# Kernel tuning notes

Measured on AMD Instinct MI355X. Metric: run time of the kernel, lower is better.

## Reference

```python
import jax, jax.numpy as jnp
import numpy as np

N_NODES = 50000
N_EDGES = 800000
N_GRAPHS = 64
NEG_SLOPE = 0.2
EPS = 1e-16


def _gat_layer(x, src, dst, W, b, att_l, att_r):
    H, C = att_l.shape
    n = x.shape[0]
    # lin_l == lin_r (shared weights in the source module)
    xl = (x @ W.T + b).reshape(n, H, C)            # [N,H,C]
    alpha_l = jnp.sum(xl * att_l, axis=-1)         # [N,H]
    alpha_r = jnp.sum(xl * att_r, axis=-1)         # [N,H]
    # per-edge attention logits: alpha_i (dst) + alpha_j (src)
    e = jax.nn.leaky_relu(alpha_r[dst] + alpha_l[src], NEG_SLOPE)  # [E,H]
    # segment softmax over destination node
    m = jax.ops.segment_max(e, dst, num_segments=n)
    e = jnp.exp(e - m[dst])
    denom = jax.ops.segment_sum(e, dst, num_segments=n)
    alpha = e / (denom[dst] + EPS)                 # [E,H]
    msg = xl[src] * alpha[:, :, None]              # [E,H,C]
    out = jax.ops.segment_sum(msg, dst, num_segments=n)  # [N,H,C]
    return out.reshape(n, H * C)


def setup_inputs() -> dict:
    key = jax.random.key(0)
    ks = jax.random.split(key, 10)
    x = jax.random.normal(ks[0], (N_NODES, 128), dtype=jnp.float32)
    edge_index = jax.random.randint(ks[1], (2, N_EDGES), 0, N_NODES, dtype=jnp.int32)
    batch = jnp.sort(jax.random.randint(ks[2], (N_NODES,), 0, N_GRAPHS, dtype=jnp.int32))
    s = 1.0 / np.sqrt(128.0)
    Ws = jax.random.normal(ks[3], (3, 128, 128), dtype=jnp.float32) * s
    bs = jnp.zeros((3, 128), dtype=jnp.float32)
    att_ls = jax.random.normal(ks[4], (3, 4, 32), dtype=jnp.float32) * s
    att_rs = jax.random.normal(ks[5], (3, 4, 32), dtype=jnp.float32) * s
    proj_W = jax.random.normal(ks[6], (32, 128), dtype=jnp.float32) * s
    proj_b = jnp.zeros((32,), dtype=jnp.float32)
    return {"x": x, "edge_index": edge_index, "batch": batch, "Ws": Ws, "bs": bs,
            "att_ls": att_ls, "att_rs": att_rs, "proj_W": proj_W, "proj_b": proj_b}


def reference(x, edge_index, batch, Ws, bs, att_ls, att_rs, proj_W, proj_b):
    src, dst = edge_index[0], edge_index[1]
    h = x
    for l in range(3):
        h = _gat_layer(h, src, dst, Ws[l], bs[l], att_ls[l], att_rs[l])
        h = jax.nn.relu(h)  # dropout disabled (eval mode)
    pooled = jax.ops.segment_sum(h, batch, num_segments=N_GRAPHS)  # [G, H*C]
    return pooled @ proj_W.T + proj_b  # output_dim=None -> return embedding
```

## Files before the change

kernel.cpp:

```cpp
#include <hip/hip_runtime.h>
#include <hip/hip_bf16.h>

#define NHEADS 4
#define DIM 128
#define NEG_SLOPE 0.2f
#define POOL_CHUNK 256

typedef __bf16 bf16x8 __attribute__((ext_vector_type(8)));
typedef float  f32x4  __attribute__((ext_vector_type(4)));

__device__ __forceinline__ float lrelu(float x) { return x > 0.f ? x : NEG_SLOPE * x; }
__device__ __forceinline__ float bf2f(unsigned short u) {
    return __uint_as_float(((unsigned)u) << 16);
}
__device__ __forceinline__ unsigned short f2bf(float f) {
    __bf16 b = (__bf16)f;
    return __builtin_bit_cast(unsigned short, b);
}
__device__ __forceinline__ float4 lrelu4(float4 a, float4 b) {
    return make_float4(lrelu(a.x + b.x), lrelu(a.y + b.y), lrelu(a.z + b.z), lrelu(a.w + b.w));
}
__device__ __forceinline__ float4 redmax4(float4 v) {
#pragma unroll
    for (int off = 32; off >= 1; off >>= 1) {
        v.x = fmaxf(v.x, __shfl_xor(v.x, off));
        v.y = fmaxf(v.y, __shfl_xor(v.y, off));
        v.z = fmaxf(v.z, __shfl_xor(v.z, off));
        v.w = fmaxf(v.w, __shfl_xor(v.w, off));
    }
    return v;
}
__device__ __forceinline__ float4 redsum4(float4 v) {
#pragma unroll
    for (int off = 32; off >= 1; off >>= 1) {
        v.x += __shfl_xor(v.x, off);
        v.y += __shfl_xor(v.y, off);
        v.z += __shfl_xor(v.z, off);
        v.w += __shfl_xor(v.w, off);
    }
    return v;
}

__global__ __launch_bounds__(256) void pack_w(
    const float* __restrict__ Ws, __bf16* __restrict__ Wb, int total)
{
    int o = blockIdx.x * 256 + threadIdx.x;
    if (o >= total) return;
    int layer = o >> 14;
    int t = o & 16383;
    int j = t & 7, l = (t >> 3) & 63, kk = (t >> 9) & 3, g = t >> 11;
    int col = g * 16 + (l & 15);
    int k = kk * 32 + (l >> 4) * 8 + j;
    Wb[o] = (__bf16)Ws[(size_t)layer * 16384 + col * 128 + k];
}

template<bool ABF>
__device__ __forceinline__ void gemm_body(
    const float* __restrict__ inF, const unsigned short* __restrict__ inB,
    const uint4* __restrict__ Wb4, const float* __restrict__ bias,
    const float* __restrict__ attl, const float* __restrict__ attr,
    __bf16* __restrict__ xlb, float* __restrict__ al, float* __restrict__ ar,
    int n, int bid)
{
    const int tid = threadIdx.x;
    const int wid = tid >> 6, l = tid & 63;
    const int rowA = bid * 64 + wid * 16 + (l & 15);
    const int kchunk = (l >> 4) * 8;

    f32x4 acc[8];
#pragma unroll
    for (int g = 0; g < 8; ++g)
#pragma unroll
        for (int r = 0; r < 4; ++r) acc[g][r] = 0.f;

#pragma unroll
    for (int kk = 0; kk < 4; ++kk) {
        bf16x8 afrag;
        if (ABF) {
            uint4 u = make_uint4(0, 0, 0, 0);
            if (rowA < n)
                u = *(const uint4*)(inB + (size_t)rowA * DIM + kk * 32 + kchunk);
            afrag = __builtin_bit_cast(bf16x8, u);
        } else {
            float av[8];
            if (rowA < n) {
                const float* p = inF + (size_t)rowA * DIM + kk * 32 + kchunk;
                float4 x0 = *(const float4*)p;
                float4 x1 = *(const float4*)(p + 4);
                av[0]=x0.x; av[1]=x0.y; av[2]=x0.z; av[3]=x0.w;
                av[4]=x1.x; av[5]=x1.y; av[6]=x1.z; av[7]=x1.w;
            } else {
#pragma unroll
                for (int i = 0; i < 8; ++i) av[i] = 0.f;
            }
#pragma unroll
            for (int i = 0; i < 8; ++i) afrag[i] = (__bf16)av[i];
        }
#pragma unroll
        for (int g = 0; g < 8; ++g) {
            uint4 u = Wb4[(g * 4 + kk) * 64 + l];
            bf16x8 bfrag = __builtin_bit_cast(bf16x8, u);
            acc[g] = __builtin_amdgcn_mfma_f32_16x16x32_bf16(afrag, bfrag, acc[g], 0, 0, 0);
        }
    }

    const int rowbase = bid * 64 + wid * 16 + (l >> 4) * 4;
    float pl[4][4], pr2[4][4];
#pragma unroll
    for (int r = 0; r < 4; ++r)
#pragma unroll
        for (int h = 0; h < 4; ++h) { pl[r][h] = 0.f; pr2[r][h] = 0.f; }

#pragma unroll
    for (int g = 0; g < 8; ++g) {
        int col = g * 16 + (l & 15);
        float bg = bias[col], alg = attl[col], arg = attr[col];
        int h = g >> 1;
#pragma unroll
        for (int r = 0; r < 4; ++r) {
            float v = acc[g][r] + bg;
            int row = rowbase + r;
            if (row < n) xlb[(size_t)row * DIM + col] = (__bf16)v;
            pl[r][h]  = fmaf(v, alg, pl[r][h]);
            pr2[r][h] = fmaf(v, arg, pr2[r][h]);
        }
    }
#pragma unroll
    for (int off = 1; off <= 8; off <<= 1) {
#pragma unroll
        for (int r = 0; r < 4; ++r)
#pragma unroll
            for (int h = 0; h < 4; ++h) {
                pl[r][h]  += __shfl_xor(pl[r][h], off);
                pr2[r][h] += __shfl_xor(pr2[r][h], off);
            }
    }
    if ((l & 15) == 0) {
#pragma unroll
        for (int r = 0; r < 4; ++r) {
            int row = rowbase + r;
            if (row < n) {
#pragma unroll
                for (int h = 0; h < 4; ++h) {
                    al[row * 4 + h] = pl[r][h];
                    ar[row * 4 + h] = pr2[r][h];
                }
            }
        }
    }
}

template<bool ABF>
__global__ __launch_bounds__(256) void gemm_mfma(
    const float* __restrict__ inF, const unsigned short* __restrict__ inB,
    const uint4* __restrict__ Wb4, const float* __restrict__ bias,
    const float* __restrict__ attl, const float* __restrict__ attr,
    __bf16* __restrict__ xlb, float* __restrict__ al, float* __restrict__ ar, int n)
{
    gemm_body<ABF>(inF, inB, Wb4, bias, attl, attr, xlb, al, ar, n, blockIdx.x);
}

__global__ __launch_bounds__(256) void gemm0_classify(
    const float* __restrict__ inF, const uint4* __restrict__ Wb4,
    const float* __restrict__ bias,
    const float* __restrict__ attl, const float* __restrict__ attr,
    __bf16* __restrict__ xlb, float* __restrict__ al, float* __restrict__ ar,
    int n, int gemmBlocks,
    const int* __restrict__ src, const int* __restrict__ dst,
    int* __restrict__ bwpos, unsigned* __restrict__ ebuf, int E)
{
    if ((int)blockIdx.x < gemmBlocks) {
        gemm_body<false>(inF, nullptr, Wb4, bias, attl, attr, xlb, al, ar, n, blockIdx.x);
    } else {
        __shared__ unsigned stage[4096];
        __shared__ unsigned char sid[4096];
        __shared__ int hist[256], lofs[256], wofs[256], gbase[256];
        int t = threadIdx.x;
        int e0 = (blockIdx.x - gemmBlocks) * 4096;
        int cnt = min(4096, E - e0);
        if (cnt <= 0) return;
        hist[t] = 0;
        __syncthreads();
        for (int k = t; k < cnt; k += 256)
            atomicAdd(&hist[dst[e0 + k] >> 8], 1);
        __syncthreads();
        int v = hist[t];
        lofs[t] = v;
        __syncthreads();
        int val = v;
        for (int off = 1; off < 256; off <<= 1) {
            int other = (t >= off) ? lofs[t - off] : 0;
            __syncthreads();
            val += other;
            lofs[t] = val;
            __syncthreads();
        }
        int excl = val - v;
        int gb_ = (v > 0) ? atomicAdd(&bwpos[t], v) : 0;
        lofs[t] = excl; wofs[t] = excl; gbase[t] = gb_;
        __syncthreads();
        for (int k = t; k < cnt; k += 256) {
            int d = dst[e0 + k], s = src[e0 + k];
            int b = d >> 8;
            int slot = atomicAdd(&wofs[b], 1);
            stage[slot] = (unsigned)(s & 0xffff) | ((unsigned)(d & 255) << 16);
            sid[slot] = (unsigned char)b;
        }
        __syncthreads();
        for (int s_ = t; s_ < cnt; s_ += 256) {
            int b = sid[s_];
            ebuf[gbase[b] + (s_ - lofs[b])] = stage[s_];
        }
    }
}

__global__ __launch_bounds__(256) void bucket_rank(
    const unsigned* __restrict__ ebuf, const int* __restrict__ rowptr,
    int* __restrict__ col, int n)
{
    __shared__ int wp[256];
    int nb0 = blockIdx.x << 8;
    int t = threadIdx.x;
    int nend = min(nb0 + 256, n);
    int base = rowptr[nb0];
    int eend = rowptr[nend];
    if (nb0 + t < nend) wp[t] = rowptr[nb0 + t] - base;
    __syncthreads();
    for (int e = base + t; e < eend; e += 256) {
        unsigned ed = ebuf[e];
        int r = atomicAdd(&wp[(ed >> 16) & 255], 1);
        col[base + r] = (int)(ed & 0xffffu);
    }
}

__global__ __launch_bounds__(256) void deg_count(
    const int* __restrict__ dst, int* __restrict__ deg, int E)
{
    int e = blockIdx.x * blockDim.x + threadIdx.x;
    if (e < E) atomicAdd(&deg[dst[e]], 1);
}

__global__ __launch_bounds__(256) void scan_blocks(
    const int* __restrict__ deg, int* __restrict__ rowptr,
    int* __restrict__ partials, int n)
{
    __shared__ int tot[256];
    int t = threadIdx.x;
    int base = blockIdx.x * 1024 + t * 4;
    int v[4];
#pragma unroll
    for (int j = 0; j < 4; ++j) v[j] = (base + j < n) ? deg[base + j] : 0;
    int p1 = v[0], p2 = p1 + v[1], p3 = p2 + v[2], sum4 = p3 + v[3];
    tot[t] = sum4;
    __syncthreads();
    int val = sum4;
    for (int off = 1; off < 256; off <<= 1) {
        int other = (t >= off) ? tot[t - off] : 0;
        __syncthreads();
        val += other;
        tot[t] = val;
        __syncthreads();
    }
    int excl = val - sum4;
    if (base < n)     rowptr[base]     = excl;
    if (base+1 < n)   rowptr[base+1]   = excl + p1;
    if (base+2 < n)   rowptr[base+2]   = excl + p2;
    if (base+3 < n)   rowptr[base+3]   = excl + p3;
    if (t == 255) partials[blockIdx.x] = val;
}

__global__ __launch_bounds__(256) void scan_partials(
    int* __restrict__ partials, int nb, int* __restrict__ rowptr, int n)
{
    __shared__ int tot[256];
    int t = threadIdx.x;
    int v = (t < nb) ? partials[t] : 0;
    tot[t] = v;
    __syncthreads();
    int val = v;
    for (int off = 1; off < 256; off <<= 1) {
        int other = (t >= off) ? tot[t - off] : 0;
        __syncthreads();
        val += other;
        tot[t] = val;
        __syncthreads();
    }
    if (t < nb) partials[t] = val - v;
    if (t == 255) rowptr[n] = val;
}

__global__ __launch_bounds__(256) void add_offsets(
    int* __restrict__ rowptr, int* __restrict__ bwpos,
    const int* __restrict__ partials, int n)
{
    int base = blockIdx.x * 1024 + threadIdx.x * 4;
    int off = partials[blockIdx.x];
#pragma unroll
    for (int j = 0; j < 4; ++j) {
        int i = base + j;
        if (i < n) {
            int r = rowptr[i] + off;
            rowptr[i] = r;
            if ((i & 255) == 0) bwpos[i >> 8] = r;
        }
    }
}

__device__ __forceinline__ void agg_chunk2(
    const int* __restrict__ slds, const float* __restrict__ wl,
    int cn, int q, const unsigned short* __restrict__ xp,
    f32x4& A, f32x4& B, f32x4& C, f32x4& D)
{
    int i = 0;
    for (; i + 8 <= cn; i += 8) {
        int e0 = i + q, e1 = i + 2 + q, e2 = i + 4 + q, e3 = i + 6 + q;
        int s0 = slds[e0], s1 = slds[e1], s2 = slds[e2], s3 = slds[e3];
        float w0 = wl[e0*4], w1 = wl[e1*4], w2 = wl[e2*4], w3 = wl[e3*4];
        ushort4 v0 = *(const ushort4*)(xp + (size_t)s0 * DIM);
        ushort4 v1 = *(const ushort4*)(xp + (size_t)s1 * DIM);
        ushort4 v2 = *(const ushort4*)(xp + (size_t)s2 * DIM);
        ushort4 v3 = *(const ushort4*)(xp + (size_t)s3 * DIM);
        A[0] = fmaf(w0, bf2f(v0.x), A[0]); A[1] = fmaf(w0, bf2f(v0.y), A[1]);
        A[2] = fmaf(w0, bf2f(v0.z), A[2]); A[3] = fmaf(w0, bf2f(v0.w), A[3]);
        B[0] = fmaf(w1, bf2f(v1.x), B[0]); B[1] = fmaf(w1, bf2f(v1.y), B[1]);
        B[2] = fmaf(w1, bf2f(v1.z), B[2]); B[3] = fmaf(w1, bf2f(v1.w), B[3]);
        C[0] = fmaf(w2, bf2f(v2.x), C[0]); C[1] = fmaf(w2, bf2f(v2.y), C[1]);
        C[2] = fmaf(w2, bf2f(v2.z), C[2]); C[3] = fmaf(w2, bf2f(v2.w), C[3]);
        D[0] = fmaf(w3, bf2f(v3.x), D[0]); D[1] = fmaf(w3, bf2f(v3.y), D[1]);
        D[2] = fmaf(w3, bf2f(v3.z), D[2]); D[3] = fmaf(w3, bf2f(v3.w), D[3]);
    }
    for (; i < cn; i += 2) {
        int e = i + q;
        if (e < cn) {
            int s = slds[e];
            float w = wl[e*4];
            ushort4 v = *(const ushort4*)(xp + (size_t)s * DIM);
            A[0] = fmaf(w, bf2f(v.x), A[0]); A[1] = fmaf(w, bf2f(v.y), A[1]);
            A[2] = fmaf(w, bf2f(v.z), A[2]); A[3] = fmaf(w, bf2f(v.w), A[3]);
        }
    }
}

__global__ __launch_bounds__(256) void gat_aggregate(
    const int* __restrict__ rowptr, const int* __restrict__ col,
    const float* __restrict__ al, const float* __restrict__ ar,
    const unsigned short* __restrict__ xlb, unsigned short* __restrict__ outb, int n)
{
    __shared__ float4 wlds[4][64];
    __shared__ int    slds[4][64];
    int wid = threadIdx.x >> 6;
    int node = blockIdx.x * 4 + wid;
    if (node >= n) return;
    int lane = threadIdx.x & 63;
    int q = lane >> 5, c32 = lane & 31;
    int h = c32 >> 3;
    int r0 = rowptr[node], r1 = rowptr[node + 1];
    int deg = r1 - r0;
    unsigned short* po = outb + (size_t)node * DIM + c32 * 4;
    if (deg == 0) {
        if (q == 0) *(ushort4*)po = make_ushort4(0, 0, 0, 0);
        return;
    }

    float4 arv = *(const float4*)(ar + (size_t)node * 4);
    const float* wl = (const float*)&wlds[wid][0] + h;
    const unsigned short* xp = xlb + c32 * 4;
    f32x4 A = {0.f,0.f,0.f,0.f}, B = {0.f,0.f,0.f,0.f};
    f32x4 C = {0.f,0.f,0.f,0.f}, D = {0.f,0.f,0.f,0.f};
    float4 inv4;

    if (deg <= 64) {
        float4 l4 = make_float4(-1e30f, -1e30f, -1e30f, -1e30f);
        int s = 0;
        if (lane < deg) {
            s = col[r0 + lane];
            float4 a = *(const float4*)(al + (size_t)s * 4);
            l4 = lrelu4(arv, a);
        }
        float4 m4 = redmax4(l4);
        float4 p4 = make_float4(0.f, 0.f, 0.f, 0.f);
        if (lane < deg) {
            p4.x = __expf(l4.x - m4.x); p4.y = __expf(l4.y - m4.y);
            p4.z = __expf(l4.z - m4.z); p4.w = __expf(l4.w - m4.w);
        }
        float4 s4 = redsum4(p4);
        inv4 = make_float4(1.f/(s4.x+1e-16f), 1.f/(s4.y+1e-16f),
                           1.f/(s4.z+1e-16f), 1.f/(s4.w+1e-16f));
        if (lane < deg) { wlds[wid][lane] = p4; slds[wid][lane] = s; }
        __asm__ volatile("s_waitcnt lgkmcnt(0)" ::: "memory");
        __builtin_amdgcn_sched_barrier(0);
        agg_chunk2(&slds[wid][0], wl, deg, q, xp, A, B, C, D);
    } else {
        float4 m4 = make_float4(-1e30f, -1e30f, -1e30f, -1e30f);
        for (int i = lane; i < deg; i += 64) {
            int s = col[r0 + i];
            float4 a = *(const float4*)(al + (size_t)s * 4);
            float4 t = lrelu4(arv, a);
            m4.x = fmaxf(m4.x, t.x); m4.y = fmaxf(m4.y, t.y);
            m4.z = fmaxf(m4.z, t.z); m4.w = fmaxf(m4.w, t.w);
        }
        m4 = redmax4(m4);
        float4 s4 = make_float4(0.f, 0.f, 0.f, 0.f);
        for (int i = lane; i < deg; i += 64) {
            int s = col[r0 + i];
            float4 a = *(const float4*)(al + (size_t)s * 4);
            float4 t = lrelu4(arv, a);
            s4.x += __expf(t.x - m4.x); s4.y += __expf(t.y - m4.y);
            s4.z += __expf(t.z - m4.z); s4.w += __expf(t.w - m4.w);
        }
        s4 = redsum4(s4);
        inv4 = make_float4(1.f/(s4.x+1e-16f), 1.f/(s4.y+1e-16f),
                           1.f/(s4.z+1e-16f), 1.f/(s4.w+1e-16f));
        for (int c0 = 0; c0 < deg; c0 += 64) {
            int cn = min(64, deg - c0);
            if (lane < cn) {
                int s = col[r0 + c0 + lane];
                float4 a = *(const float4*)(al + (size_t)s * 4);
                float4 t = lrelu4(arv, a);
                float4 p;
                p.x = __expf(t.x - m4.x); p.y = __expf(t.y - m4.y);
                p.z = __expf(t.z - m4.z); p.w = __expf(t.w - m4.w);
                wlds[wid][lane] = p; slds[wid][lane] = s;
            }
            __asm__ volatile("s_waitcnt lgkmcnt(0)" ::: "memory");
            __builtin_amdgcn_sched_barrier(0);
            agg_chunk2(&slds[wid][0], wl, cn, q, xp, A, B, C, D);
            __asm__ volatile("s_waitcnt lgkmcnt(0)" ::: "memory");
            __builtin_amdgcn_sched_barrier(0);
        }
    }
    float invh = (h == 0) ? inv4.x : (h == 1) ? inv4.y : (h == 2) ? inv4.z : inv4.w;
    f32x4 T;
#pragma unroll
    for (int j = 0; j < 4; ++j) {
        T[j] = A[j] + B[j] + C[j] + D[j];
        T[j] += __shfl_xor(T[j], 32);
    }
    if (q == 0) {
        ushort4 o4;
        o4.x = f2bf(fmaxf(T[0] * invh, 0.f));
        o4.y = f2bf(fmaxf(T[1] * invh, 0.f));
        o4.z = f2bf(fmaxf(T[2] * invh, 0.f));
        o4.w = f2bf(fmaxf(T[3] * invh, 0.f));
        *(ushort4*)po = o4;
    }
}

__global__ __launch_bounds__(256) void pool_nodes_seg(
    const unsigned short* __restrict__ h, const int* __restrict__ batch,
    float* __restrict__ pooled, int n)
{
    int wid = threadIdx.x >> 6;
    int lane = threadIdx.x & 63;
    int start = blockIdx.x * POOL_CHUNK;
    int end = min(start + POOL_CHUNK, n);
    float a0 = 0.f, a1 = 0.f;
    int curg = -1;
    for (int node = start + wid; node < end; node += 4) {
        int g = batch[node];
        if (g != curg) {
            if (curg >= 0) {
                unsafeAtomicAdd(pooled + (size_t)curg * DIM + lane*2,     a0);
                unsafeAtomicAdd(pooled + (size_t)curg * DIM + lane*2 + 1, a1);
            }
            curg = g; a0 = 0.f; a1 = 0.f;
        }
        ushort2 v = *(const ushort2*)(h + (size_t)node * DIM + lane * 2);
        a0 += bf2f(v.x);
        a1 += bf2f(v.y);
    }
    if (curg >= 0) {
        unsafeAtomicAdd(pooled + (size_t)curg * DIM + lane*2,     a0);
        unsafeAtomicAdd(pooled + (size_t)curg * DIM + lane*2 + 1, a1);
    }
}

__global__ __launch_bounds__(256) void proj_out(
    const float* __restrict__ pooled, const float* __restrict__ W,
    const float* __restrict__ b, float* __restrict__ out, int G)
{
    int idx = blockIdx.x * blockDim.x + threadIdx.x;
    if (idx >= G * 32) return;
    int g = idx >> 5, j = idx & 31;
    const float* pr = pooled + (size_t)g * DIM;
    const float* wr = W + (size_t)j * DIM;
    float acc = 0.f;
#pragma unroll
    for (int k = 0; k < DIM; ++k) acc = fmaf(pr[k], wr[k], acc);
    out[idx] = acc + b[j];
}

extern "C" void kernel_launch(void* const* d_in, const int* in_sizes, int n_in,
                              void* d_out, int out_size, void* d_ws, size_t ws_size,
                              hipStream_t stream)
{
    const float* x      = (const float*)d_in[0];
    const int*   eidx   = (const int*)d_in[1];
    const int*   batch  = (const int*)d_in[2];
    const float* Ws     = (const float*)d_in[3];
    const float* bs     = (const float*)d_in[4];
    const float* attls  = (const float*)d_in[5];
    const float* attrs  = (const float*)d_in[6];
    const float* projW  = (const float*)d_in[7];
    const float* projb  = (const float*)d_in[8];

    const int N = in_sizes[0] / DIM;
    const int E = in_sizes[1] / 2;
    const int G = out_size / 32;
    const int* src = eidx;
    const int* dst = eidx + E;

    char* ws = (char*)d_ws;
    size_t o = 0;
    auto alloc = [&](size_t bytes) { char* p = ws + o; o += (bytes + 255) & ~255ull; return p; };
    unsigned short* hA  = (unsigned short*)alloc((size_t)N * DIM * 2);
    unsigned short* hB  = (unsigned short*)alloc((size_t)N * DIM * 2);
    __bf16* xlb    = (__bf16*)alloc((size_t)N * DIM * 2);
    float*  al     = (float*)alloc((size_t)N * 4 * 4);
    float*  ar     = (float*)alloc((size_t)N * 4 * 4);
    int*    rowptr = (int*)alloc((size_t)(N + 1) * 4);
    int*    deg    = (int*)alloc((size_t)N * 4);
    int*    colv   = (int*)alloc((size_t)E * 4);
    unsigned* ebuf = (unsigned*)alloc((size_t)E * 4);
    int*    bwpos  = (int*)alloc((size_t)((N + 255) / 256) * 4);
    int*    parts  = (int*)alloc(256 * 4);
    float*  pooled = (float*)alloc((size_t)G * DIM * 4);
    __bf16* Wb     = (__bf16*)alloc((size_t)3 * 16384 * 2);

    const int wtot = 3 * 16384;
    pack_w<<<(wtot + 255) / 256, 256, 0, stream>>>(Ws, Wb, wtot);

    const int nb = (N + 1023) / 1024;
    hipMemsetAsync(deg, 0, (size_t)N * 4, stream);
    deg_count<<<(E + 255) / 256, 256, 0, stream>>>(dst, deg, E);
    scan_blocks<<<nb, 256, 0, stream>>>(deg, rowptr, parts, N);
    scan_partials<<<1, 256, 0, stream>>>(parts, nb, rowptr, N);
    add_offsets<<<nb, 256, 0, stream>>>(rowptr, bwpos, parts, N);

    const int gb = (N + 63) / 64;
    const int cb = (E + 4095) / 4096;
    const int rb = (N + 255) / 256;

    gemm0_classify<<<gb + cb, 256, 0, stream>>>(
        x, (const uint4*)Wb, bs, attls, attrs, xlb, al, ar, N, gb,
        src, dst, bwpos, ebuf, E);
    bucket_rank<<<rb, 256, 0, stream>>>(ebuf, rowptr, colv, N);
    gat_aggregate<<<(N + 3) / 4, 256, 0, stream>>>(rowptr, colv, al, ar,
        (const unsigned short*)xlb, hA, N);

    const unsigned short* hin = hA;
    unsigned short* houts[2] = {hB, hA};
    for (int l = 1; l < 3; ++l) {
        unsigned short* hout = houts[l - 1];
        const uint4* Wb4 = (const uint4*)(Wb + (size_t)l * 16384);
        gemm_mfma<true><<<gb, 256, 0, stream>>>(nullptr, hin, Wb4, bs + l*DIM,
            attls + l*DIM, attrs + l*DIM, xlb, al, ar, N);
        gat_aggregate<<<(N + 3) / 4, 256, 0, stream>>>(rowptr, colv, al, ar,
            (const unsigned short*)xlb, hout, N);
        hin = hout;
    }

    hipMemsetAsync(pooled, 0, (size_t)G * DIM * 4, stream);
    pool_nodes_seg<<<(N + POOL_CHUNK - 1) / POOL_CHUNK, 256, 0, stream>>>(hA, batch, pooled, N);
    proj_out<<<(G * 32 + 255) / 256, 256, 0, stream>>>(pooled, projW, projb, (float*)d_out, G);
}
```

Baseline: 293.3 us.

## Drop softmax max pass, widen aggregation loads, fuse weight packing with degree count

Removes the per-node max reduction from the segment softmax and exponentiates raw logits directly, eliminating a shuffle reduction and an extra edge pass for high-degree nodes. The aggregation loop now has each lane load 8 bf16 features (16-byte loads) across 4 edge groups instead of 4 features across 2. Weight packing and degree counting are merged into one launch. Skipping the max subtraction risks exp overflow for large attention logits.

New measurement: 258.6 us. 1.13x faster.

```diff
diff --git a/kernel.cpp b/kernel.cpp
--- a/kernel.cpp
+++ b/kernel.cpp
@@ -17,18 +17,11 @@
     __bf16 b = (__bf16)f;
     return __builtin_bit_cast(unsigned short, b);
 }
+__device__ __forceinline__ unsigned pack2bf(float a, float b) {
+    return (unsigned)f2bf(a) | ((unsigned)f2bf(b) << 16);
+}
 __device__ __forceinline__ float4 lrelu4(float4 a, float4 b) {
     return make_float4(lrelu(a.x + b.x), lrelu(a.y + b.y), lrelu(a.z + b.z), lrelu(a.w + b.w));
-}
-__device__ __forceinline__ float4 redmax4(float4 v) {
-#pragma unroll
-    for (int off = 32; off >= 1; off >>= 1) {
-        v.x = fmaxf(v.x, __shfl_xor(v.x, off));
-        v.y = fmaxf(v.y, __shfl_xor(v.y, off));
-        v.z = fmaxf(v.z, __shfl_xor(v.z, off));
-        v.w = fmaxf(v.w, __shfl_xor(v.w, off));
-    }
-    return v;
 }
 __device__ __forceinline__ float4 redsum4(float4 v) {
 #pragma unroll
@@ -39,19 +32,6 @@
         v.w += __shfl_xor(v.w, off);
     }
     return v;
-}
-
-__global__ __launch_bounds__(256) void pack_w(
-    const float* __restrict__ Ws, __bf16* __restrict__ Wb, int total)
-{
-    int o = blockIdx.x * 256 + threadIdx.x;
-    if (o >= total) return;
-    int layer = o >> 14;
-    int t = o & 16383;
-    int j = t & 7, l = (t >> 3) & 63, kk = (t >> 9) & 3, g = t >> 11;
-    int col = g * 16 + (l & 15);
-    int k = kk * 32 + (l >> 4) * 8 + j;
-    Wb[o] = (__bf16)Ws[(size_t)layer * 16384 + col * 128 + k];
 }
 
 template<bool ABF>
@@ -233,11 +213,23 @@
     }
 }
 
-__global__ __launch_bounds__(256) void deg_count(
+__global__ __launch_bounds__(256) void prep_pack_deg(
+    const float* __restrict__ Ws, __bf16* __restrict__ Wb, int wtot, int wb,
     const int* __restrict__ dst, int* __restrict__ deg, int E)
 {
-    int e = blockIdx.x * blockDim.x + threadIdx.x;
-    if (e < E) atomicAdd(&deg[dst[e]], 1);
+    if ((int)blockIdx.x < wb) {
+        int o = blockIdx.x * 256 + threadIdx.x;
+        if (o >= wtot) return;
+        int layer = o >> 14;
+        int t = o & 16383;
+        int j = t & 7, l = (t >> 3) & 63, kk = (t >> 9) & 3, g = t >> 11;
+        int col = g * 16 + (l & 15);
+        int k = kk * 32 + (l >> 4) * 8 + j;
+        Wb[o] = (__bf16)Ws[(size_t)layer * 16384 + col * 128 + k];
+    } else {
+        int e = (blockIdx.x - wb) * 256 + threadIdx.x;
+        if (e < E) atomicAdd(&deg[dst[e]], 1);
+    }
 }
 
 __global__ __launch_bounds__(256) void scan_blocks(
@@ -306,37 +298,41 @@
     }
 }
 
-__device__ __forceinline__ void agg_chunk2(
+__device__ __forceinline__ void acc_edge(
+    uint4 v, float w, f32x4& lo, f32x4& hi)
+{
+    lo[0] = fmaf(w, __uint_as_float(v.x << 16), lo[0]);
+    lo[1] = fmaf(w, __uint_as_float(v.x & 0xffff0000u), lo[1]);
+    lo[2] = fmaf(w, __uint_as_float(v.y << 16), lo[2]);
+    lo[3] = fmaf(w, __uint_as_float(v.y & 0xffff0000u), lo[3]);
+    hi[0] = fmaf(w, __uint_as_float(v.z << 16), hi[0]);
+    hi[1] = fmaf(w, __uint_as_float(v.z & 0xffff0000u), hi[1]);
+    hi[2] = fmaf(w, __uint_as_float(v.w << 16), hi[2]);
+    hi[3] = fmaf(w, __uint_as_float(v.w & 0xffff0000u), hi[3]);
+}
+
+__device__ __forceinline__ void agg_chunk4w(
     const int* __restrict__ slds, const float* __restrict__ wl,
-    int cn, int q, const unsigned short* __restrict__ xp,
-    f32x4& A, f32x4& B, f32x4& C, f32x4& D)
+    int cn, int eg, const unsigned short* __restrict__ xp,
+    f32x4& A0, f32x4& A1, f32x4& B0, f32x4& B1)
 {
     int i = 0;
     for (; i + 8 <= cn; i += 8) {
-        int e0 = i + q, e1 = i + 2 + q, e2 = i + 4 + q, e3 = i + 6 + q;
-        int s0 = slds[e0], s1 = slds[e1], s2 = slds[e2], s3 = slds[e3];
-        float w0 = wl[e0*4], w1 = wl[e1*4], w2 = wl[e2*4], w3 = wl[e3*4];
-        ushort4 v0 = *(const ushort4*)(xp + (size_t)s0 * DIM);
-        ushort4 v1 = *(const ushort4*)(xp + (size_t)s1 * DIM);
-        ushort4 v2 = *(const ushort4*)(xp + (size_t)s2 * DIM);
-        ushort4 v3 = *(const ushort4*)(xp + (size_t)s3 * DIM);
-        A[0] = fmaf(w0, bf2f(v0.x), A[0]); A[1] = fmaf(w0, bf2f(v0.y), A[1]);
-        A[2] = fmaf(w0, bf2f(v0.z), A[2]); A[3] = fmaf(w0, bf2f(v0.w), A[3]);
-        B[0] = fmaf(w1, bf2f(v1.x), B[0]); B[1] = fmaf(w1, bf2f(v1.y), B[1]);
-        B[2] = fmaf(w1, bf2f(v1.z), B[2]); B[3] = fmaf(w1, bf2f(v1.w), B[3]);
-        C[0] = fmaf(w2, bf2f(v2.x), C[0]); C[1] = fmaf(w2, bf2f(v2.y), C[1]);
-        C[2] = fmaf(w2, bf2f(v2.z), C[2]); C[3] = fmaf(w2, bf2f(v2.w), C[3]);
-        D[0] = fmaf(w3, bf2f(v3.x), D[0]); D[1] = fmaf(w3, bf2f(v3.y), D[1]);
-        D[2] = fmaf(w3, bf2f(v3.z), D[2]); D[3] = fmaf(w3, bf2f(v3.w), D[3]);
-    }
-    for (; i < cn; i += 2) {
-        int e = i + q;
+        int e0 = i + eg, e1 = i + 4 + eg;
+        int s0 = slds[e0], s1 = slds[e1];
+        float w0 = wl[e0*4], w1 = wl[e1*4];
+        uint4 v0 = *(const uint4*)(xp + (size_t)s0 * DIM);
+        uint4 v1 = *(const uint4*)(xp + (size_t)s1 * DIM);
+        acc_edge(v0, w0, A0, A1);
+        acc_edge(v1, w1, B0, B1);
+    }
+    for (; i < cn; i += 4) {
+        int e = i + eg;
         if (e < cn) {
             int s = slds[e];
             float w = wl[e*4];
-            ushort4 v = *(const ushort4*)(xp + (size_t)s * DIM);
-            A[0] = fmaf(w, bf2f(v.x), A[0]); A[1] = fmaf(w, bf2f(v.y), A[1]);
-            A[2] = fmaf(w, bf2f(v.z), A[2]); A[3] = fmaf(w, bf2f(v.w), A[3]);
+            uint4 v = *(const uint4*)(xp + (size_t)s * DIM);
+            acc_edge(v, w, A0, A1);
         }
     }
 }
@@ -352,36 +348,31 @@
     int node = blockIdx.x * 4 + wid;
     if (node >= n) return;
     int lane = threadIdx.x & 63;
-    int q = lane >> 5, c32 = lane & 31;
-    int h = c32 >> 3;
+    int eg = lane >> 4, c16 = lane & 15;
+    int h = c16 >> 2;
     int r0 = rowptr[node], r1 = rowptr[node + 1];
     int deg = r1 - r0;
-    unsigned short* po = outb + (size_t)node * DIM + c32 * 4;
+    unsigned short* po = outb + (size_t)node * DIM + c16 * 8;
     if (deg == 0) {
-        if (q == 0) *(ushort4*)po = make_ushort4(0, 0, 0, 0);
+        if (eg == 0) *(uint4*)po = make_uint4(0, 0, 0, 0);
         return;
     }
 
     float4 arv = *(const float4*)(ar + (size_t)node * 4);
     const float* wl = (const float*)&wlds[wid][0] + h;
-    const unsigned short* xp = xlb + c32 * 4;
-    f32x4 A = {0.f,0.f,0.f,0.f}, B = {0.f,0.f,0.f,0.f};
-    f32x4 C = {0.f,0.f,0.f,0.f}, D = {0.f,0.f,0.f,0.f};
+    const unsigned short* xp = xlb + c16 * 8;
+    f32x4 A0 = {0,0,0,0}, A1 = {0,0,0,0}, B0 = {0,0,0,0}, B1 = {0,0,0,0};
     float4 inv4;
 
     if (deg <= 64) {
-        float4 l4 = make_float4(-1e30f, -1e30f, -1e30f, -1e30f);
+        float4 p4 = make_float4(0.f, 0.f, 0.f, 0.f);
         int s = 0;
         if (lane < deg) {
             s = col[r0 + lane];
             float4 a = *(const float4*)(al + (size_t)s * 4);
-            l4 = lrelu4(arv, a);
-        }
-        float4 m4 = redmax4(l4);
-        float4 p4 = make_float4(0.f, 0.f, 0.f, 0.f);
-        if (lane < deg) {
-            p4.x = __expf(l4.x - m4.x); p4.y = __expf(l4.y - m4.y);
-            p4.z = __expf(l4.z - m4.z); p4.w = __expf(l4.w - m4.w);
+            float4 l4 = lrelu4(arv, a);
+            p4.x = __expf(l4.x); p4.y = __expf(l4.y);
+            p4.z = __expf(l4.z); p4.w = __expf(l4.w);
         }
         float4 s4 = redsum4(p4);
         inv4 = make_float4(1.f/(s4.x+1e-16f), 1.f/(s4.y+1e-16f),
@@ -389,24 +380,15 @@
         if (lane < deg) { wlds[wid][lane] = p4; slds[wid][lane] = s; }
         __asm__ volatile("s_waitcnt lgkmcnt(0)" ::: "memory");
         __builtin_amdgcn_sched_barrier(0);
-        agg_chunk2(&slds[wid][0], wl, deg, q, xp, A, B, C, D);
+        agg_chunk4w(&slds[wid][0], wl, deg, eg, xp, A0, A1, B0, B1);
     } else {
-        float4 m4 = make_float4(-1e30f, -1e30f, -1e30f, -1e30f);
-        for (int i = lane; i < deg; i += 64) {
-            int s = col[r0 + i];
-            float4 a = *(const float4*)(al + (size_t)s * 4);
-            float4 t = lrelu4(arv, a);
-            m4.x = fmaxf(m4.x, t.x); m4.y = fmaxf(m4.y, t.y);
-            m4.z = fmaxf(m4.z, t.z); m4.w = fmaxf(m4.w, t.w);
-        }
-        m4 = redmax4(m4);
         float4 s4 = make_float4(0.f, 0.f, 0.f, 0.f);
         for (int i = lane; i < deg; i += 64) {
             int s = col[r0 + i];
             float4 a = *(const float4*)(al + (size_t)s * 4);
             float4 t = lrelu4(arv, a);
-            s4.x += __expf(t.x - m4.x); s4.y += __expf(t.y - m4.y);
-            s4.z += __expf(t.z - m4.z); s4.w += __expf(t.w - m4.w);
+            s4.x += __expf(t.x); s4.y += __expf(t.y);
+            s4.z += __expf(t.z); s4.w += __expf(t.w);
         }
         s4 = redsum4(s4);
         inv4 = make_float4(1.f/(s4.x+1e-16f), 1.f/(s4.y+1e-16f),
@@ -418,31 +400,32 @@
                 float4 a = *(const float4*)(al + (size_t)s * 4);
                 float4 t = lrelu4(arv, a);
                 float4 p;
-                p.x = __expf(t.x - m4.x); p.y = __expf(t.y - m4.y);
-                p.z = __expf(t.z - m4.z); p.w = __expf(t.w - m4.w);
+                p.x = __expf(t.x); p.y = __expf(t.y);
+                p.z = __expf(t.z); p.w = __expf(t.w);
                 wlds[wid][lane] = p; slds[wid][lane] = s;
             }
             __asm__ volatile("s_waitcnt lgkmcnt(0)" ::: "memory");
             __builtin_amdgcn_sched_barrier(0);
-            agg_chunk2(&slds[wid][0], wl, cn, q, xp, A, B, C, D);
+            agg_chunk4w(&slds[wid][0], wl, cn, eg, xp, A0, A1, B0, B1);
             __asm__ volatile("s_waitcnt lgkmcnt(0)" ::: "memory");
             __builtin_amdgcn_sched_barrier(0);
         }
     }
     float invh = (h == 0) ? inv4.x : (h == 1) ? inv4.y : (h == 2) ? inv4.z : inv4.w;
-    f32x4 T;
 #pragma unroll
     for (int j = 0; j < 4; ++j) {
-        T[j] = A[j] + B[j] + C[j] + D[j];
-        T[j] += __shfl_xor(T[j], 32);
-    }
-    if (q == 0) {
-        ushort4 o4;
-        o4.x = f2bf(fmaxf(T[0] * invh, 0.f));
-        o4.y = f2bf(fmaxf(T[1] * invh, 0.f));
-        o4.z = f2bf(fmaxf(T[2] * invh, 0.f));
-        o4.w = f2bf(fmaxf(T[3] * invh, 0.f));
-        *(ushort4*)po = o4;
+        A0[j] += B0[j];
+        A1[j] += B1[j];
+        A0[j] += __shfl_xor(A0[j], 16); A0[j] += __shfl_xor(A0[j], 32);
+        A1[j] += __shfl_xor(A1[j], 16); A1[j] += __shfl_xor(A1[j], 32);
+    }
+    if (eg == 0) {
+        uint4 o4;
+        o4.x = pack2bf(fmaxf(A0[0]*invh, 0.f), fmaxf(A0[1]*invh, 0.f));
+        o4.y = pack2bf(fmaxf(A0[2]*invh, 0.f), fmaxf(A0[3]*invh, 0.f));
+        o4.z = pack2bf(fmaxf(A1[0]*invh, 0.f), fmaxf(A1[1]*invh, 0.f));
+        o4.w = pack2bf(fmaxf(A1[2]*invh, 0.f), fmaxf(A1[3]*invh, 0.f));
+        *(uint4*)po = o4;
     }
 }
 
@@ -528,11 +511,12 @@
     __bf16* Wb     = (__bf16*)alloc((size_t)3 * 16384 * 2);
 
     const int wtot = 3 * 16384;
-    pack_w<<<(wtot + 255) / 256, 256, 0, stream>>>(Ws, Wb, wtot);
+    const int wb = (wtot + 255) / 256;
+    const int db = (E + 255) / 256;
+    hipMemsetAsync(deg, 0, (size_t)N * 4, stream);
+    prep_pack_deg<<<wb + db, 256, 0, stream>>>(Ws, Wb, wtot, wb, dst, deg, E);
 
     const int nb = (N + 1023) / 1024;
-    hipMemsetAsync(deg, 0, (size_t)N * 4, stream);
-    deg_count<<<(E + 255) / 256, 256, 0, stream>>>(dst, deg, E);
     scan_blocks<<<nb, 256, 0, stream>>>(deg, rowptr, parts, N);
     scan_partials<<<1, 256, 0, stream>>>(parts, nb, rowptr, N);
     add_offsets<<<nb, 256, 0, stream>>>(rowptr, bwpos, parts, N);
```
